# Optimization experiments

Measured on AMD Instinct MI355X. Metric: run time of the kernel, lower is better.

## Reference

```python
import jax, jax.numpy as jnp
import numpy as np

HIDDEN_NF = 256
ATOMICA_DIM = 512
NUM_HEADS = 4
HEAD_DIM = HIDDEN_NF // NUM_HEADS
EDGE_CUTOFF = 10.0
N_LIG = 1024
N_POCKET = 8192
BOX = 30.0  # Angstrom box so the cutoff mask is selective


def _lin(key, fan_in, fan_out):
    kw, kb = jax.random.split(key)
    s = 1.0 / np.sqrt(fan_in)
    W = jax.random.uniform(kw, (fan_in, fan_out), jnp.float32, -s, s)
    b = jax.random.uniform(kb, (fan_out,), jnp.float32, -s, s)
    return W, b


def setup_inputs() -> dict:
    key = jax.random.key(0)
    ks = jax.random.split(key, 12)
    h_lig = jax.random.normal(ks[0], (N_LIG, HIDDEN_NF), jnp.float32)
    x_lig = jax.random.uniform(ks[1], (N_LIG, 3), jnp.float32) * BOX
    h_atomica = jax.random.normal(ks[2], (N_POCKET, ATOMICA_DIM), jnp.float32)
    x_pocket = jax.random.uniform(ks[3], (N_POCKET, 3), jnp.float32) * BOX
    qw, qb = _lin(ks[4], HIDDEN_NF, HIDDEN_NF)
    kw, kb = _lin(ks[5], ATOMICA_DIM, HIDDEN_NF)
    vw, vb = _lin(ks[6], ATOMICA_DIM, HIDDEN_NF)
    ow, ob = _lin(ks[7], HIDDEN_NF, HIDDEN_NF)
    e1w, e1b = _lin(ks[8], 1, HIDDEN_NF)
    e2w, e2b = _lin(ks[9], HIDDEN_NF, NUM_HEADS)
    c1w, c1b = _lin(ks[10], HIDDEN_NF, HIDDEN_NF)
    c2w, c2b = _lin(ks[11], HIDDEN_NF, 1)
    return dict(h_lig=h_lig, x_lig=x_lig, h_atomica=h_atomica, x_pocket=x_pocket,
                qw=qw, qb=qb, kw=kw, kb=kb, vw=vw, vb=vb, ow=ow, ob=ob,
                e1w=e1w, e1b=e1b, e2w=e2w, e2b=e2b,
                c1w=c1w, c1b=c1b, c2w=c2w, c2b=c2b)


def reference(h_lig, x_lig, h_atomica, x_pocket,
              qw, qb, kw, kb, vw, vb, ow, ob,
              e1w, e1b, e2w, e2b, c1w, c1b, c2w, c2b):
    N_lig = h_lig.shape[0]
    silu = jax.nn.silu
    # pairwise geometry: [N_lig, N_pocket, 3]
    rel_pos = x_pocket[None, :, :] - x_lig[:, None, :]
    distances = jnp.linalg.norm(rel_pos, axis=-1, keepdims=True)  # [Nl,Np,1]
    # edge bias MLP: [Nl,Np,num_heads]
    edge_attr = silu(distances @ e1w + e1b) @ e2w + e2b
    mask = distances[..., 0] < EDGE_CUTOFF  # [Nl,Np]
    Q = (h_lig @ qw + qb).reshape(N_lig, NUM_HEADS, HEAD_DIM)
    K = (h_atomica @ kw + kb).reshape(-1, NUM_HEADS, HEAD_DIM)
    V = (h_atomica @ vw + vb).reshape(-1, NUM_HEADS, HEAD_DIM)
    scores = jnp.einsum('ihd,jhd->ijh', Q, K) / np.sqrt(HEAD_DIM).astype(np.float32)
    scores = scores + edge_attr
    scores = jnp.where(mask[..., None], scores, -jnp.inf)
    attn = jax.nn.softmax(scores, axis=1)
    attn = jnp.where(jnp.isnan(attn), 0.0, attn)  # nan_to_num for fully-masked rows
    h_attended = jnp.einsum('ijh,jhd->ihd', attn, V).reshape(N_lig, HIDDEN_NF)
    h_out = h_lig + h_attended @ ow + ob
    # equivariant coordinate update
    normalized_rel_pos = rel_pos / (distances + 1e-8)
    avg_attn = attn.mean(axis=-1, keepdims=True)  # [Nl,Np,1]
    coord_messages = (avg_attn * normalized_rel_pos).sum(axis=1)  # [Nl,3]
    coord_scale = silu(h_attended @ c1w + c1b) @ c2w + c2b  # [Nl,1]
    x_out = x_lig + coord_scale * coord_messages
    return h_out, x_out
```

## Files before the change

kernel.cpp:

```cpp
#include <hip/hip_runtime.h>
#include <hip/hip_bf16.h>


#define NLIG   1024
#define NPOCK  8192
#define HIDDEN 256
#define ADIM   512
#define NHEAD  4
#define HDIM   64
#define NTAB   1024
#define NSPLIT 16
#define CHUNK  (NPOCK / NSPLIT)
#define NT     (CHUNK / 32)
#define LOG2E  1.4426950408889634f
#define QK_SCALE (0.125f * LOG2E)

typedef float f32x16 __attribute__((ext_vector_type(16)));
typedef short short8 __attribute__((ext_vector_type(8)));

union U4S8 { uint4 u; short8 s; };

static __device__ __forceinline__ float exp2h(float x) {
  float r; asm("v_exp_f32 %0, %1" : "=v"(r) : "v"(x)); return r;
}
static __device__ __forceinline__ float rsqh(float x) {
  float r; asm("v_rsq_f32 %0, %1" : "=v"(r) : "v"(x)); return r;
}
static __device__ __forceinline__ unsigned cvtpk(float lo, float hi) {
  unsigned r;
  asm("v_cvt_pk_bf16_f32 %0, %1, %2" : "=v"(r) : "v"(lo), "v"(hi));
  return r;
}
static __device__ __forceinline__ unsigned short f2bf(float f) {
  union { __hip_bfloat16 h; unsigned short u; } c;
  c.h = __float2bfloat16(f);
  return c.u;
}
static __device__ __forceinline__ float bf2f(unsigned u16) {
  union { unsigned uu; float f; } c;
  c.uu = u16 << 16;
  return c.f;
}
static __device__ __forceinline__ short8 load_bf8(const unsigned short* p) {
  U4S8 t; t.u = *(const uint4*)p; return t.s;
}
static __device__ __forceinline__ f32x16 mfma32(short8 a, short8 b, f32x16 c) {
  return __builtin_amdgcn_mfma_f32_32x32x16_bf16(a, b, c, 0, 0, 0);
}
static __device__ __forceinline__ size_t t8(int r, int c, int Cdiv8) {
  return ((size_t)((r >> 5) * Cdiv8 + (c >> 3)) << 8) + ((r & 31) << 3) + (c & 7);
}

#define NCAST 4352
#define NTRANS 448
__global__ __launch_bounds__(256)
void prep_kernel(const float* __restrict__ hA, const float* __restrict__ hl,
                 const float* __restrict__ qw, const float* __restrict__ kw,
                 const float* __restrict__ vw, const float* __restrict__ ow,
                 const float* __restrict__ c1w,
                 const float* __restrict__ e1w, const float* __restrict__ e1b,
                 const float* __restrict__ e2w, const float* __restrict__ e2b,
                 unsigned short* __restrict__ hAb, unsigned short* __restrict__ hlb,
                 unsigned short* __restrict__ qwT, unsigned short* __restrict__ kwT,
                 unsigned short* __restrict__ vwT, unsigned short* __restrict__ owT,
                 unsigned short* __restrict__ c1wT, float* __restrict__ tabG) {
  int bx = blockIdx.x;
  int tid = threadIdx.x;
  if (bx < NCAST) {
    int id = bx * 256 + tid;
    const int nA4 = NPOCK * ADIM / 4;
    if (id < nA4) {
      float4 v = ((const float4*)hA)[id];
      int r = id >> 7, c0 = (id << 2) & 511;
      ushort4 o; o.x = f2bf(v.x); o.y = f2bf(v.y); o.z = f2bf(v.z); o.w = f2bf(v.w);
      *(ushort4*)(hAb + t8(r, c0, 64)) = o;
    } else {
      int j = id - nA4;
      float4 v = ((const float4*)hl)[j];
      int r = j >> 6, c0 = (j << 2) & 255;
      ushort4 o; o.x = f2bf(v.x); o.y = f2bf(v.y); o.z = f2bf(v.z); o.w = f2bf(v.w);
      *(ushort4*)(hlb + t8(r, c0, 32)) = o;
    }
  } else if (bx < NCAST + NTRANS) {
    int b = bx - NCAST;
    const float* src; unsigned short* dst; int K;
    if (b < 64)       { src = qw;  dst = qwT;  K = 256; }
    else if (b < 192) { src = kw;  dst = kwT;  K = 512; b -= 64; }
    else if (b < 320) { src = vw;  dst = vwT;  K = 512; b -= 192; }
    else if (b < 384) { src = ow;  dst = owT;  K = 256; b -= 320; }
    else              { src = c1w; dst = c1wT; K = 256; b -= 384; }
    int kt = K / 32;
    int k0 = (b % kt) * 32, n0 = (b / kt) * 32;
    __shared__ float tile[32][33];
    int tx = tid & 31, ty = tid >> 5;
#pragma unroll
    for (int r = 0; r < 4; ++r)
      tile[ty + 8 * r][tx] = src[(k0 + ty + 8 * r) * 256 + n0 + tx];
    __syncthreads();
#pragma unroll
    for (int r = 0; r < 4; ++r)
      dst[t8(n0 + ty + 8 * r, k0 + tx, K >> 3)] = f2bf(tile[tx][ty + 8 * r]);
  } else {
    int eb = bx - (NCAST + NTRANS);
    int w = tid >> 6, l = tid & 63;
    int entry = eb * 4 + w;
    float d = (entry + 0.5f) * (10.0f / NTAB);
    float a0 = 0.f, a1 = 0.f, a2 = 0.f, a3 = 0.f;
#pragma unroll
    for (int jj = 0; jj < 4; ++jj) {
      int j = l + jj * 64;
      float v = fmaf(d, e1w[j], e1b[j]);
      float s = v / (1.0f + __expf(-v));
      float4 w2 = ((const float4*)e2w)[j];
      a0 = fmaf(s, w2.x, a0);
      a1 = fmaf(s, w2.y, a1);
      a2 = fmaf(s, w2.z, a2);
      a3 = fmaf(s, w2.w, a3);
    }
#pragma unroll
    for (int m = 32; m >= 1; m >>= 1) {
      a0 += __shfl_xor(a0, m); a1 += __shfl_xor(a1, m);
      a2 += __shfl_xor(a2, m); a3 += __shfl_xor(a3, m);
    }
    if (l == 0) {
      tabG[0 * NTAB + entry] = (a0 + e2b[0]) * LOG2E;
      tabG[1 * NTAB + entry] = (a1 + e2b[1]) * LOG2E;
      tabG[2 * NTAB + entry] = (a2 + e2b[2]) * LOG2E;
      tabG[3 * NTAB + entry] = (a3 + e2b[3]) * LOG2E;
    }
  }
}

__global__ __launch_bounds__(256)
void proj_kernel(const unsigned short* __restrict__ hAb, const unsigned short* __restrict__ hlb,
                 const unsigned short* __restrict__ kwT, const unsigned short* __restrict__ vwT,
                 const unsigned short* __restrict__ qwT,
                 const float* __restrict__ kb, const float* __restrict__ vb,
                 const float* __restrict__ qb,
                 unsigned short* __restrict__ Kb, unsigned short* __restrict__ VTb,
                 unsigned short* __restrict__ Qb) {
  int tid = threadIdx.x;
  int w = tid >> 6, lane = tid & 63;
  int lo = lane & 31, hi = lane >> 5;
  int n0 = blockIdx.y * 32;
  int n = n0 + lo;
  if (blockIdx.x < 64) {
    int m0 = blockIdx.x * 128 + w * 32;
    const unsigned short* ap  = hAb + t8(m0 + lo, hi * 8, 64);
    const unsigned short* bkp = kwT + t8(n, hi * 8, 64);
    const unsigned short* bvp = vwT + t8(n, hi * 8, 64);
    f32x16 aK, aV;
#pragma unroll
    for (int i = 0; i < 16; ++i) { aK[i] = 0.f; aV[i] = 0.f; }
#pragma unroll 8
    for (int kk = 0; kk < ADIM / 16; ++kk) {
      short8 a  = load_bf8(ap + kk * 512);
      short8 bk = load_bf8(bkp + kk * 512);
      short8 bv = load_bf8(bvp + kk * 512);
      aK = mfma32(a, bk, aK);
      aV = mfma32(bv, a, aV);
    }
    float bnK = kb[n];
#pragma unroll
    for (int g = 0; g < 4; ++g) {
#pragma unroll
      for (int rr = 0; rr < 4; ++rr) {
        int r = g * 4 + rr;
        int row = g * 8 + hi * 4 + rr;
        Kb[t8(m0 + row, n, 32)] = f2bf(aK[r] + bnK);
        int nv = n0 + row;
        VTb[t8(nv, m0 + lo, 1024)] = f2bf(aV[r] + vb[nv]);
      }
    }
  } else {
    int m0 = (blockIdx.x - 64) * 128 + w * 32;
    const unsigned short* ap = hlb + t8(m0 + lo, hi * 8, 32);
    const unsigned short* bp = qwT + t8(n, hi * 8, 32);
    f32x16 acc;
#pragma unroll
    for (int i = 0; i < 16; ++i) acc[i] = 0.f;
#pragma unroll 8
    for (int kk = 0; kk < HIDDEN / 16; ++kk) {
      short8 a = load_bf8(ap + kk * 512);
      short8 b = load_bf8(bp + kk * 512);
      acc = mfma32(a, b, acc);
    }
    float bn = qb[n];
#pragma unroll
    for (int g = 0; g < 4; ++g) {
#pragma unroll
      for (int rr = 0; rr < 4; ++rr) {
        int r = g * 4 + rr;
        int m = m0 + g * 8 + hi * 4 + rr;
        Qb[t8(m, n, 32)] = f2bf(acc[r] + bn);
      }
    }
  }
}

__global__ __launch_bounds__(256)
void attn_kernel(const unsigned short* __restrict__ Qbf, const unsigned short* __restrict__ Kbf,
                 const unsigned short* __restrict__ VTbf,
                 const float* __restrict__ x_lig, const float* __restrict__ x_pocket,
                 const float* __restrict__ tabG,
                 unsigned* __restrict__ partOb, float4* __restrict__ partZC) {
  __shared__ float4 xch[CHUNK];
  __shared__ float tab[NHEAD][NTAB];

  int tid = threadIdx.x;
  int h = tid >> 6;
  int lane = tid & 63;
  int lo = lane & 31, hi = lane >> 5;
  int qt = blockIdx.x & 31;
  int split = blockIdx.x >> 5;
  int q0 = qt * 32;
  int j0g = split * CHUNK;

  for (int i = tid; i < CHUNK; i += 256) {
    float x = x_pocket[(j0g + i) * 3 + 0];
    float y = x_pocket[(j0g + i) * 3 + 1];
    float z = x_pocket[(j0g + i) * 3 + 2];
    float4 v; v.x = x; v.y = y; v.z = z; v.w = 0.f;
    xch[i] = v;
  }
  for (int i = tid; i < NHEAD * NTAB; i += 256) ((float*)tab)[i] = tabG[i];
  __syncthreads();

  int q = q0 + lo;
  float xl0 = x_lig[q * 3 + 0];
  float xl1 = x_lig[q * 3 + 1];
  float xl2 = x_lig[q * 3 + 2];

  short8 qfr[4];
#pragma unroll
  for (int kk = 0; kk < 4; ++kk)
    qfr[kk] = load_bf8(Qbf + t8(q, h * HDIM + kk * 16 + hi * 8, 32));

  const unsigned short* kbp = Kbf + t8(j0g + lo, h * HDIM + hi * 8, 32);
  const unsigned short* vbp = VTbf + t8(h * HDIM + lo, j0g + hi * 8, 1024);

  f32x16 O0, O1;
#pragma unroll
  for (int i = 0; i < 16; ++i) { O0[i] = 0.f; O1[i] = 0.f; }
  float Z = 0.f, c0 = 0.f, c1 = 0.f, c2 = 0.f;

  short8 kcur[4];
#pragma unroll
  for (int kk = 0; kk < 4; ++kk) kcur[kk] = load_bf8(kbp + kk * 512);

#pragma unroll 1
  for (int t = 0; t < NT; ++t) {
    int jb = t * 32;
    int tn = (t + 1 < NT) ? (t + 1) : t;
    short8 knx0 = load_bf8(kbp + (size_t)tn * 8192 + 0 * 512);
    short8 knx1 = load_bf8(kbp + (size_t)tn * 8192 + 1 * 512);
    short8 knx2 = load_bf8(kbp + (size_t)tn * 8192 + 2 * 512);
    short8 knx3 = load_bf8(kbp + (size_t)tn * 8192 + 3 * 512);
    short8 v00 = load_bf8(vbp + (size_t)t * 1024);
    short8 v01 = load_bf8(vbp + (size_t)t * 1024 + 262144);
    short8 v10 = load_bf8(vbp + (size_t)t * 1024 + 512);
    short8 v11 = load_bf8(vbp + (size_t)t * 1024 + 512 + 262144);

    f32x16 s;
#pragma unroll
    for (int i = 0; i < 16; ++i) s[i] = 0.f;
    s = mfma32(kcur[0], qfr[0], s);
    s = mfma32(kcur[1], qfr[1], s);
    s = mfma32(kcur[2], qfr[2], s);
    s = mfma32(kcur[3], qfr[3], s);

    unsigned wp[8];
    float pprev = 0.f;
#pragma unroll
    for (int r = 0; r < 16; ++r) {
      int jl = (r & 3) + 8 * (r >> 2) + 4 * hi;
      float4 xp = xch[jb + jl];
      float dx = xp.x - xl0, dy = xp.y - xl1, dz = xp.z - xl2;
      float r2 = fmaf(dx, dx, fmaf(dy, dy, dz * dz));
      float r2c = fmaxf(r2, 1e-24f);
      float rinv = rsqh(r2c);
      float d = r2c * rinv;
      int idx = (int)(d * (NTAB / 10.0f));
      idx = idx > (NTAB - 1) ? (NTAB - 1) : idx;
      float b = tab[h][idx];
      float s2 = fmaf(s[r], QK_SCALE, b);
      float pe = (r2 < 100.0f) ? exp2h(s2) : 0.0f;
      Z += pe;
      float pr = pe * rinv;
      c0 = fmaf(pr, dx, c0);
      c1 = fmaf(pr, dy, c1);
      c2 = fmaf(pr, dz, c2);
      if (r & 1) wp[r >> 1] = cvtpk(pprev, pe); else pprev = pe;
    }
    {
      unsigned W0 = wp[0], W1 = wp[1], W2 = wp[2], W3 = wp[3];
      unsigned e01 = (unsigned)__shfl_xor((int)(hi ? W0 : W2), 32);
      unsigned e23 = (unsigned)__shfl_xor((int)(hi ? W1 : W3), 32);
      U4S8 pb;
      pb.u.x = hi ? e01 : W0;
      pb.u.y = hi ? e23 : W1;
      pb.u.z = hi ? W2 : e01;
      pb.u.w = hi ? W3 : e23;
      O0 = mfma32(v00, pb.s, O0);
      O1 = mfma32(v01, pb.s, O1);
    }
    {
      unsigned W0 = wp[4], W1 = wp[5], W2 = wp[6], W3 = wp[7];
      unsigned e01 = (unsigned)__shfl_xor((int)(hi ? W0 : W2), 32);
      unsigned e23 = (unsigned)__shfl_xor((int)(hi ? W1 : W3), 32);
      U4S8 pb;
      pb.u.x = hi ? e01 : W0;
      pb.u.y = hi ? e23 : W1;
      pb.u.z = hi ? W2 : e01;
      pb.u.w = hi ? W3 : e23;
      O0 = mfma32(v10, pb.s, O0);
      O1 = mfma32(v11, pb.s, O1);
    }
    kcur[0] = knx0; kcur[1] = knx1; kcur[2] = knx2; kcur[3] = knx3;
  }

  unsigned* po = partOb + ((size_t)(split * NLIG + q) * (HIDDEN / 2)) + h * (HDIM / 2);
#pragma unroll
  for (int g = 0; g < 4; ++g) {
    uint2 u0;
    u0.x = cvtpk(O0[g * 4 + 0], O0[g * 4 + 1]);
    u0.y = cvtpk(O0[g * 4 + 2], O0[g * 4 + 3]);
    *(uint2*)(po + g * 4 + hi * 2) = u0;
    uint2 u1;
    u1.x = cvtpk(O1[g * 4 + 0], O1[g * 4 + 1]);
    u1.y = cvtpk(O1[g * 4 + 2], O1[g * 4 + 3]);
    *(uint2*)(po + 16 + g * 4 + hi * 2) = u1;
  }
  float Zt = Z + __shfl_xor(Z, 32);
  float c0t = c0 + __shfl_xor(c0, 32);
  float c1t = c1 + __shfl_xor(c1, 32);
  float c2t = c2 + __shfl_xor(c2, 32);
  if (hi == 0) {
    float4 zc; zc.x = Zt; zc.y = c0t; zc.z = c1t; zc.w = c2t;
    partZC[(size_t)(split * NLIG + q) * NHEAD + h] = zc;
  }
}

__global__ __launch_bounds__(256)
void combine_kernel(const unsigned short* __restrict__ partOb, const float4* __restrict__ partZC,
                    unsigned short* __restrict__ hattb, float* __restrict__ cmsg) {
  int q = blockIdx.x;
  int t = threadIdx.x;
  int h = t >> 6;
  float Zh = 0.f;
#pragma unroll
  for (int s = 0; s < NSPLIT; ++s) Zh += partZC[(size_t)(s * NLIG + q) * NHEAD + h].x;
  float o = 0.f;
#pragma unroll
  for (int s = 0; s < NSPLIT; ++s)
    o += bf2f(partOb[(size_t)(s * NLIG + q) * HIDDEN + t]);
  float inv = (Zh > 0.f) ? 1.0f / Zh : 0.f;
  hattb[t8(q, t, 32)] = f2bf(o * inv);

  __shared__ float sm[NHEAD][3];
  if (t < NHEAD) {
    float zz = 0.f, a0 = 0.f, a1 = 0.f, a2 = 0.f;
    for (int s = 0; s < NSPLIT; ++s) {
      float4 v = partZC[(size_t)(s * NLIG + q) * NHEAD + t];
      zz += v.x; a0 += v.y; a1 += v.z; a2 += v.w;
    }
    float iv = (zz > 0.f) ? 0.25f / zz : 0.f;
    sm[t][0] = a0 * iv; sm[t][1] = a1 * iv; sm[t][2] = a2 * iv;
  }
  __syncthreads();
  if (t < 3) cmsg[q * 3 + t] = sm[0][t] + sm[1][t] + sm[2][t] + sm[3][t];
}

__global__ __launch_bounds__(256)
void epi_kernel(const unsigned short* __restrict__ hatt,
                const unsigned short* __restrict__ owT, const unsigned short* __restrict__ c1wT,
                const float* __restrict__ ob, const float* __restrict__ c1b,
                const float* __restrict__ c2w, const float* __restrict__ h_lig,
                float* __restrict__ hout, float* __restrict__ cscale) {
  int tid = threadIdx.x;
  int w = tid >> 6, lane = tid & 63;
  int lo = lane & 31, hi = lane >> 5;
  int m0 = blockIdx.x * 128 + w * 32;
  int n0 = blockIdx.y * 32;
  int n = n0 + lo;
  const unsigned short* ap = hatt + t8(m0 + lo, hi * 8, 32);
  const unsigned short* bo = owT + t8(n, hi * 8, 32);
  const unsigned short* bc = c1wT + t8(n, hi * 8, 32);
  f32x16 aO, aC;
#pragma unroll
  for (int i = 0; i < 16; ++i) { aO[i] = 0.f; aC[i] = 0.f; }
#pragma unroll 8
  for (int kk = 0; kk < HIDDEN / 16; ++kk) {
    short8 a  = load_bf8(ap + kk * 512);
    short8 b1 = load_bf8(bo + kk * 512);
    short8 b2 = load_bf8(bc + kk * 512);
    aO = mfma32(a, b1, aO);
    aC = mfma32(a, b2, aC);
  }
  float obn = ob[n], c1bn = c1b[n], c2wn = c2w[n];
#pragma unroll
  for (int g = 0; g < 4; ++g) {
#pragma unroll
    for (int rr = 0; rr < 4; ++rr) {
      int r = g * 4 + rr;
      int m = m0 + g * 8 + hi * 4 + rr;
      hout[(size_t)m * HIDDEN + n] = aO[r] + obn + h_lig[(size_t)m * HIDDEN + n];
      float v = aC[r] + c1bn;
      float sg = v / (1.0f + exp2h(-LOG2E * v));
      float part = sg * c2wn;
#pragma unroll
      for (int msk = 16; msk >= 1; msk >>= 1) part += __shfl_xor(part, msk);
      if (lo == 0) atomicAdd(&cscale[m], part);
    }
  }
}

__global__ __launch_bounds__(256)
void coordfin_kernel(const float* __restrict__ cscale, const float* __restrict__ c2b,
                     const float* __restrict__ cmsg, const float* __restrict__ x_lig,
                     float* __restrict__ x_out) {
  int id = blockIdx.x * 256 + threadIdx.x;
  if (id < NLIG * 3) {
    int q = id / 3;
    x_out[id] = x_lig[id] + (cscale[q] + c2b[0]) * cmsg[id];
  }
}

extern "C" void kernel_launch(void* const* d_in, const int* in_sizes, int n_in,
                              void* d_out, int out_size, void* d_ws, size_t ws_size,
                              hipStream_t stream) {
  const float* h_lig  = (const float*)d_in[0];
  const float* x_lig  = (const float*)d_in[1];
  const float* h_atom = (const float*)d_in[2];
  const float* x_pock = (const float*)d_in[3];
  const float* qw  = (const float*)d_in[4];
  const float* qb  = (const float*)d_in[5];
  const float* kw  = (const float*)d_in[6];
  const float* kb  = (const float*)d_in[7];
  const float* vw  = (const float*)d_in[8];
  const float* vb  = (const float*)d_in[9];
  const float* ow  = (const float*)d_in[10];
  const float* ob  = (const float*)d_in[11];
  const float* e1w = (const float*)d_in[12];
  const float* e1b = (const float*)d_in[13];
  const float* e2w = (const float*)d_in[14];
  const float* e2b = (const float*)d_in[15];
  const float* c1w = (const float*)d_in[16];
  const float* c1b = (const float*)d_in[17];
  const float* c2w = (const float*)d_in[18];
  const float* c2b = (const float*)d_in[19];

  char* w = (char*)d_ws;
  unsigned short* hAb  = (unsigned short*)w; w += (size_t)NPOCK * ADIM * 2;
  unsigned short* hlb  = (unsigned short*)w; w += (size_t)NLIG * HIDDEN * 2;
  unsigned short* qwT  = (unsigned short*)w; w += 256 * 256 * 2;
  unsigned short* kwT  = (unsigned short*)w; w += 256 * 512 * 2;
  unsigned short* vwT  = (unsigned short*)w; w += 256 * 512 * 2;
  unsigned short* owT  = (unsigned short*)w; w += 256 * 256 * 2;
  unsigned short* c1wT = (unsigned short*)w; w += 256 * 256 * 2;
  unsigned short* Qb   = (unsigned short*)w; w += (size_t)NLIG * HIDDEN * 2;
  unsigned short* Kb   = (unsigned short*)w; w += (size_t)NPOCK * HIDDEN * 2;
  unsigned short* VTb  = (unsigned short*)w; w += (size_t)HIDDEN * NPOCK * 2;
  float* tabG          = (float*)w;          w += NHEAD * NTAB * 4;
  unsigned* partOb     = (unsigned*)w;       w += (size_t)NSPLIT * NLIG * HIDDEN * 2;
  float* partZC        = (float*)w;          w += (size_t)NSPLIT * NLIG * NHEAD * 4 * 4;
  unsigned short* hatt = (unsigned short*)w; w += (size_t)NLIG * HIDDEN * 2;
  float* cmsg          = (float*)w;          w += (size_t)NLIG * 3 * 4;
  float* cscale        = (float*)w;          w += (size_t)NLIG * 4;

  float* hout = (float*)d_out;
  float* xout = ((float*)d_out) + (size_t)NLIG * HIDDEN;

  prep_kernel<<<NCAST + NTRANS + NTAB / 4, 256, 0, stream>>>(
      h_atom, h_lig, qw, kw, vw, ow, c1w, e1w, e1b, e2w, e2b,
      hAb, hlb, qwT, kwT, vwT, owT, c1wT, tabG);
  proj_kernel<<<dim3(72, 8), 256, 0, stream>>>(
      hAb, hlb, kwT, vwT, qwT, kb, vb, qb, Kb, VTb, Qb);
  attn_kernel<<<32 * NSPLIT, 256, 0, stream>>>(Qb, Kb, VTb, x_lig, x_pock, tabG,
                                               partOb, (float4*)partZC);
  combine_kernel<<<NLIG, 256, 0, stream>>>((const unsigned short*)partOb,
                                           (const float4*)partZC, hatt, cmsg);
  hipMemsetAsync(cscale, 0, NLIG * sizeof(float), stream);
  epi_kernel<<<dim3(8, 8), 256, 0, stream>>>(hatt, owT, c1wT, ob, c1b, c2w, h_lig,
                                             hout, cscale);
  coordfin_kernel<<<(NLIG * 3 + 255) / 256, 256, 0, stream>>>(cscale, c2b, cmsg,
                                                              x_lig, xout);
}
```

Baseline: 182.7 us.

## Fuse combine, epilogue and coord kernels; widen projection tiles; tile input cast

```diff
diff --git a/kernel.cpp b/kernel.cpp
--- a/kernel.cpp
+++ b/kernel.cpp
@@ -51,7 +51,8 @@
   return ((size_t)((r >> 5) * Cdiv8 + (c >> 3)) << 8) + ((r & 31) << 3) + (c & 7);
 }
 
-#define NCAST 4352
+#define NCASTA 1024
+#define NCASTL 64
 #define NTRANS 448
 __global__ __launch_bounds__(256)
 void prep_kernel(const float* __restrict__ hA, const float* __restrict__ hl,
@@ -66,23 +67,40 @@
                  unsigned short* __restrict__ c1wT, float* __restrict__ tabG) {
   int bx = blockIdx.x;
   int tid = threadIdx.x;
-  if (bx < NCAST) {
-    int id = bx * 256 + tid;
-    const int nA4 = NPOCK * ADIM / 4;
-    if (id < nA4) {
-      float4 v = ((const float4*)hA)[id];
-      int r = id >> 7, c0 = (id << 2) & 511;
-      ushort4 o; o.x = f2bf(v.x); o.y = f2bf(v.y); o.z = f2bf(v.z); o.w = f2bf(v.w);
-      *(ushort4*)(hAb + t8(r, c0, 64)) = o;
+  if (bx < NCASTA + NCASTL) {
+    const float* src; unsigned short* dst; int stride, Cdiv8, R0, C0;
+    if (bx < NCASTA) {
+      src = hA; dst = hAb; stride = ADIM; Cdiv8 = 64;
+      R0 = (bx >> 3) * 64; C0 = (bx & 7) * 64;
     } else {
-      int j = id - nA4;
-      float4 v = ((const float4*)hl)[j];
-      int r = j >> 6, c0 = (j << 2) & 255;
-      ushort4 o; o.x = f2bf(v.x); o.y = f2bf(v.y); o.z = f2bf(v.z); o.w = f2bf(v.w);
-      *(ushort4*)(hlb + t8(r, c0, 32)) = o;
-    }
-  } else if (bx < NCAST + NTRANS) {
-    int b = bx - NCAST;
+      int b = bx - NCASTA;
+      src = hl; dst = hlb; stride = HIDDEN; Cdiv8 = 32;
+      R0 = (b >> 2) * 64; C0 = (b & 3) * 64;
+    }
+    __shared__ float tf[64][65];
+    int r = tid >> 2;
+#pragma unroll
+    for (int pass = 0; pass < 4; ++pass) {
+      int c4 = (tid & 3) + pass * 4;
+      float4 v = ((const float4*)(src + (size_t)(R0 + r) * stride + C0))[c4];
+      tf[r][c4 * 4 + 0] = v.x; tf[r][c4 * 4 + 1] = v.y;
+      tf[r][c4 * 4 + 2] = v.z; tf[r][c4 * 4 + 3] = v.w;
+    }
+    __syncthreads();
+    unsigned* dstu = (unsigned*)dst;
+    size_t tbase = (size_t)(R0 >> 5) * Cdiv8 + (C0 >> 3);
+#pragma unroll
+    for (int k = 0; k < 8; ++k) {
+      int u = k * 256 + tid;
+      int tile = u >> 7, w2 = u & 127;
+      int rb = tile >> 3, cb = tile & 7;
+      int rr = rb * 32 + (w2 >> 2);
+      int c = cb * 8 + (w2 & 3) * 2;
+      unsigned val = cvtpk(tf[rr][c], tf[rr][c + 1]);
+      dstu[(tbase + (size_t)rb * Cdiv8 + cb) * 128 + w2] = val;
+    }
+  } else if (bx < NCASTA + NCASTL + NTRANS) {
+    int b = bx - (NCASTA + NCASTL);
     const float* src; unsigned short* dst; int K;
     if (b < 64)       { src = qw;  dst = qwT;  K = 256; }
     else if (b < 192) { src = kw;  dst = kwT;  K = 512; b -= 64; }
@@ -101,7 +119,7 @@
     for (int r = 0; r < 4; ++r)
       dst[t8(n0 + ty + 8 * r, k0 + tx, K >> 3)] = f2bf(tile[tx][ty + 8 * r]);
   } else {
-    int eb = bx - (NCAST + NTRANS);
+    int eb = bx - (NCASTA + NCASTL + NTRANS);
     int w = tid >> 6, l = tid & 63;
     int entry = eb * 4 + w;
     float d = (entry + 0.5f) * (10.0f / NTAB);
@@ -142,57 +160,67 @@
   int tid = threadIdx.x;
   int w = tid >> 6, lane = tid & 63;
   int lo = lane & 31, hi = lane >> 5;
-  int n0 = blockIdx.y * 32;
-  int n = n0 + lo;
+  int n0 = blockIdx.y * 64;
   if (blockIdx.x < 64) {
     int m0 = blockIdx.x * 128 + w * 32;
-    const unsigned short* ap  = hAb + t8(m0 + lo, hi * 8, 64);
-    const unsigned short* bkp = kwT + t8(n, hi * 8, 64);
-    const unsigned short* bvp = vwT + t8(n, hi * 8, 64);
-    f32x16 aK, aV;
-#pragma unroll
-    for (int i = 0; i < 16; ++i) { aK[i] = 0.f; aV[i] = 0.f; }
-#pragma unroll 8
+    const unsigned short* ap   = hAb + t8(m0 + lo, hi * 8, 64);
+    const unsigned short* bk0p = kwT + t8(n0 + lo, hi * 8, 64);
+    const unsigned short* bk1p = bk0p + 64 * 256;
+    const unsigned short* bv0p = vwT + t8(n0 + lo, hi * 8, 64);
+    const unsigned short* bv1p = bv0p + 64 * 256;
+    f32x16 aK0, aK1, aV0, aV1;
+#pragma unroll
+    for (int i = 0; i < 16; ++i) { aK0[i] = 0.f; aK1[i] = 0.f; aV0[i] = 0.f; aV1[i] = 0.f; }
+#pragma unroll 4
     for (int kk = 0; kk < ADIM / 16; ++kk) {
-      short8 a  = load_bf8(ap + kk * 512);
-      short8 bk = load_bf8(bkp + kk * 512);
-      short8 bv = load_bf8(bvp + kk * 512);
-      aK = mfma32(a, bk, aK);
-      aV = mfma32(bv, a, aV);
-    }
-    float bnK = kb[n];
+      short8 a   = load_bf8(ap + kk * 512);
+      short8 bk0 = load_bf8(bk0p + kk * 512);
+      short8 bk1 = load_bf8(bk1p + kk * 512);
+      short8 bv0 = load_bf8(bv0p + kk * 512);
+      short8 bv1 = load_bf8(bv1p + kk * 512);
+      aK0 = mfma32(a, bk0, aK0);
+      aK1 = mfma32(a, bk1, aK1);
+      aV0 = mfma32(bv0, a, aV0);
+      aV1 = mfma32(bv1, a, aV1);
+    }
+    float bnK0 = kb[n0 + lo], bnK1 = kb[n0 + 32 + lo];
 #pragma unroll
     for (int g = 0; g < 4; ++g) {
 #pragma unroll
       for (int rr = 0; rr < 4; ++rr) {
         int r = g * 4 + rr;
         int row = g * 8 + hi * 4 + rr;
-        Kb[t8(m0 + row, n, 32)] = f2bf(aK[r] + bnK);
-        int nv = n0 + row;
-        VTb[t8(nv, m0 + lo, 1024)] = f2bf(aV[r] + vb[nv]);
+        Kb[t8(m0 + row, n0 + lo, 32)]      = f2bf(aK0[r] + bnK0);
+        Kb[t8(m0 + row, n0 + 32 + lo, 32)] = f2bf(aK1[r] + bnK1);
+        VTb[t8(n0 + row, m0 + lo, 1024)]      = f2bf(aV0[r] + vb[n0 + row]);
+        VTb[t8(n0 + 32 + row, m0 + lo, 1024)] = f2bf(aV1[r] + vb[n0 + 32 + row]);
       }
     }
   } else {
     int m0 = (blockIdx.x - 64) * 128 + w * 32;
-    const unsigned short* ap = hlb + t8(m0 + lo, hi * 8, 32);
-    const unsigned short* bp = qwT + t8(n, hi * 8, 32);
-    f32x16 acc;
-#pragma unroll
-    for (int i = 0; i < 16; ++i) acc[i] = 0.f;
+    const unsigned short* ap  = hlb + t8(m0 + lo, hi * 8, 32);
+    const unsigned short* b0p = qwT + t8(n0 + lo, hi * 8, 32);
+    const unsigned short* b1p = b0p + 32 * 256;
+    f32x16 a0, a1;
+#pragma unroll
+    for (int i = 0; i < 16; ++i) { a0[i] = 0.f; a1[i] = 0.f; }
 #pragma unroll 8
     for (int kk = 0; kk < HIDDEN / 16; ++kk) {
-      short8 a = load_bf8(ap + kk * 512);
-      short8 b = load_bf8(bp + kk * 512);
-      acc = mfma32(a, b, acc);
-    }
-    float bn = qb[n];
+      short8 a  = load_bf8(ap + kk * 512);
+      short8 b0 = load_bf8(b0p + kk * 512);
+      short8 b1 = load_bf8(b1p + kk * 512);
+      a0 = mfma32(a, b0, a0);
+      a1 = mfma32(a, b1, a1);
+    }
+    float bn0 = qb[n0 + lo], bn1 = qb[n0 + 32 + lo];
 #pragma unroll
     for (int g = 0; g < 4; ++g) {
 #pragma unroll
       for (int rr = 0; rr < 4; ++rr) {
         int r = g * 4 + rr;
         int m = m0 + g * 8 + hi * 4 + rr;
-        Qb[t8(m, n, 32)] = f2bf(acc[r] + bn);
+        Qb[t8(m, n0 + lo, 32)]      = f2bf(a0[r] + bn0);
+        Qb[t8(m, n0 + 32 + lo, 32)] = f2bf(a1[r] + bn1);
       }
     }
   }
@@ -341,61 +369,73 @@
   }
 }
 
-__global__ __launch_bounds__(256)
-void combine_kernel(const unsigned short* __restrict__ partOb, const float4* __restrict__ partZC,
-                    unsigned short* __restrict__ hattb, float* __restrict__ cmsg) {
-  int q = blockIdx.x;
+__global__ __launch_bounds__(512)
+void tail_kernel(const unsigned* __restrict__ partOb, const float4* __restrict__ partZC,
+                 const unsigned short* __restrict__ owT, const unsigned short* __restrict__ c1wT,
+                 const float* __restrict__ ob, const float* __restrict__ c1b,
+                 const float* __restrict__ c2w, const float* __restrict__ c2b,
+                 const float* __restrict__ h_lig, const float* __restrict__ x_lig,
+                 float* __restrict__ hout, float* __restrict__ xout) {
+  __shared__ unsigned hattL[32 * 128];
+  __shared__ float invL[32][4];
+  __shared__ float cmsgL[32][3];
+  __shared__ float cscL[32];
+
   int t = threadIdx.x;
-  int h = t >> 6;
-  float Zh = 0.f;
-#pragma unroll
-  for (int s = 0; s < NSPLIT; ++s) Zh += partZC[(size_t)(s * NLIG + q) * NHEAD + h].x;
-  float o = 0.f;
-#pragma unroll
-  for (int s = 0; s < NSPLIT; ++s)
-    o += bf2f(partOb[(size_t)(s * NLIG + q) * HIDDEN + t]);
-  float inv = (Zh > 0.f) ? 1.0f / Zh : 0.f;
-  hattb[t8(q, t, 32)] = f2bf(o * inv);
-
-  __shared__ float sm[NHEAD][3];
-  if (t < NHEAD) {
+  int q0 = blockIdx.x * 32;
+
+  if (t < 128) {
+    int i = t >> 2, h = t & 3;
     float zz = 0.f, a0 = 0.f, a1 = 0.f, a2 = 0.f;
+#pragma unroll
     for (int s = 0; s < NSPLIT; ++s) {
-      float4 v = partZC[(size_t)(s * NLIG + q) * NHEAD + t];
+      float4 v = partZC[(size_t)(s * NLIG + q0 + i) * NHEAD + h];
       zz += v.x; a0 += v.y; a1 += v.z; a2 += v.w;
     }
+    invL[i][h] = (zz > 0.f) ? 1.0f / zz : 0.f;
     float iv = (zz > 0.f) ? 0.25f / zz : 0.f;
-    sm[t][0] = a0 * iv; sm[t][1] = a1 * iv; sm[t][2] = a2 * iv;
-  }
+    a0 *= iv; a1 *= iv; a2 *= iv;
+    a0 += __shfl_xor(a0, 1); a0 += __shfl_xor(a0, 2);
+    a1 += __shfl_xor(a1, 1); a1 += __shfl_xor(a1, 2);
+    a2 += __shfl_xor(a2, 1); a2 += __shfl_xor(a2, 2);
+    if (h == 0) { cmsgL[i][0] = a0; cmsgL[i][1] = a1; cmsgL[i][2] = a2; }
+  }
+  if (t < 32) cscL[t] = 0.f;
   __syncthreads();
-  if (t < 3) cmsg[q * 3 + t] = sm[0][t] + sm[1][t] + sm[2][t] + sm[3][t];
-}
-
-__global__ __launch_bounds__(256)
-void epi_kernel(const unsigned short* __restrict__ hatt,
-                const unsigned short* __restrict__ owT, const unsigned short* __restrict__ c1wT,
-                const float* __restrict__ ob, const float* __restrict__ c1b,
-                const float* __restrict__ c2w, const float* __restrict__ h_lig,
-                float* __restrict__ hout, float* __restrict__ cscale) {
-  int tid = threadIdx.x;
-  int w = tid >> 6, lane = tid & 63;
+
+  {
+    int c2i = t & 127;
+    int c = c2i * 2;
+#pragma unroll
+    for (int i = t >> 7; i < 32; i += 4) {
+      float o0 = 0.f, o1 = 0.f;
+#pragma unroll
+      for (int s = 0; s < NSPLIT; ++s) {
+        unsigned u = partOb[(size_t)(s * NLIG + q0 + i) * 128 + c2i];
+        o0 += bf2f(u & 0xffffu);
+        o1 += bf2f(u >> 16);
+      }
+      float inv = invL[i][c >> 6];
+      hattL[(c >> 3) * 128 + i * 4 + ((c & 7) >> 1)] = cvtpk(o0 * inv, o1 * inv);
+    }
+  }
+  __syncthreads();
+
+  int w = t >> 6, lane = t & 63;
   int lo = lane & 31, hi = lane >> 5;
-  int m0 = blockIdx.x * 128 + w * 32;
-  int n0 = blockIdx.y * 32;
-  int n = n0 + lo;
-  const unsigned short* ap = hatt + t8(m0 + lo, hi * 8, 32);
+  int n = w * 32 + lo;
   const unsigned short* bo = owT + t8(n, hi * 8, 32);
   const unsigned short* bc = c1wT + t8(n, hi * 8, 32);
   f32x16 aO, aC;
 #pragma unroll
   for (int i = 0; i < 16; ++i) { aO[i] = 0.f; aC[i] = 0.f; }
 #pragma unroll 8
-  for (int kk = 0; kk < HIDDEN / 16; ++kk) {
-    short8 a  = load_bf8(ap + kk * 512);
+  for (int kk = 0; kk < 16; ++kk) {
+    U4S8 av; av.u = *(const uint4*)&hattL[(kk * 2 + hi) * 128 + lo * 4];
     short8 b1 = load_bf8(bo + kk * 512);
     short8 b2 = load_bf8(bc + kk * 512);
-    aO = mfma32(a, b1, aO);
-    aC = mfma32(a, b2, aC);
+    aO = mfma32(av.s, b1, aO);
+    aC = mfma32(av.s, b2, aC);
   }
   float obn = ob[n], c1bn = c1b[n], c2wn = c2w[n];
 #pragma unroll
@@ -403,26 +443,23 @@
 #pragma unroll
     for (int rr = 0; rr < 4; ++rr) {
       int r = g * 4 + rr;
-      int m = m0 + g * 8 + hi * 4 + rr;
+      int mi = g * 8 + hi * 4 + rr;
+      int m = q0 + mi;
       hout[(size_t)m * HIDDEN + n] = aO[r] + obn + h_lig[(size_t)m * HIDDEN + n];
       float v = aC[r] + c1bn;
       float sg = v / (1.0f + exp2h(-LOG2E * v));
       float part = sg * c2wn;
 #pragma unroll
       for (int msk = 16; msk >= 1; msk >>= 1) part += __shfl_xor(part, msk);
-      if (lo == 0) atomicAdd(&cscale[m], part);
-    }
-  }
-}
-
-__global__ __launch_bounds__(256)
-void coordfin_kernel(const float* __restrict__ cscale, const float* __restrict__ c2b,
-                     const float* __restrict__ cmsg, const float* __restrict__ x_lig,
-                     float* __restrict__ x_out) {
-  int id = blockIdx.x * 256 + threadIdx.x;
-  if (id < NLIG * 3) {
-    int q = id / 3;
-    x_out[id] = x_lig[id] + (cscale[q] + c2b[0]) * cmsg[id];
+      if (lo == 0) atomicAdd(&cscL[mi], part);
+    }
+  }
+  __syncthreads();
+
+  if (t < 96) {
+    int i = t / 3, d = t % 3;
+    int q = q0 + i;
+    xout[q * 3 + d] = x_lig[q * 3 + d] + (cscL[i] + c2b[0]) * cmsgL[i][d];
   }
 }
 
@@ -464,25 +501,17 @@
   float* tabG          = (float*)w;          w += NHEAD * NTAB * 4;
   unsigned* partOb     = (unsigned*)w;       w += (size_t)NSPLIT * NLIG * HIDDEN * 2;
   float* partZC        = (float*)w;          w += (size_t)NSPLIT * NLIG * NHEAD * 4 * 4;
-  unsigned short* hatt = (unsigned short*)w; w += (size_t)NLIG * HIDDEN * 2;
-  float* cmsg          = (float*)w;          w += (size_t)NLIG * 3 * 4;
-  float* cscale        = (float*)w;          w += (size_t)NLIG * 4;
 
   float* hout = (float*)d_out;
   float* xout = ((float*)d_out) + (size_t)NLIG * HIDDEN;
 
-  prep_kernel<<<NCAST + NTRANS + NTAB / 4, 256, 0, stream>>>(
+  prep_kernel<<<NCASTA + NCASTL + NTRANS + NTAB / 4, 256, 0, stream>>>(
       h_atom, h_lig, qw, kw, vw, ow, c1w, e1w, e1b, e2w, e2b,
       hAb, hlb, qwT, kwT, vwT, owT, c1wT, tabG);
-  proj_kernel<<<dim3(72, 8), 256, 0, stream>>>(
+  proj_kernel<<<dim3(72, 4), 256, 0, stream>>>(
       hAb, hlb, kwT, vwT, qwT, kb, vb, qb, Kb, VTb, Qb);
   attn_kernel<<<32 * NSPLIT, 256, 0, stream>>>(Qb, Kb, VTb, x_lig, x_pock, tabG,
                                                partOb, (float4*)partZC);
-  combine_kernel<<<NLIG, 256, 0, stream>>>((const unsigned short*)partOb,
-                                           (const float4*)partZC, hatt, cmsg);
-  hipMemsetAsync(cscale, 0, NLIG * sizeof(float), stream);
-  epi_kernel<<<dim3(8, 8), 256, 0, stream>>>(hatt, owT, c1wT, ob, c1b, c2w, h_lig,
-                                             hout, cscale);
-  coordfin_kernel<<<(NLIG * 3 + 255) / 256, 256, 0, stream>>>(cscale, c2b, cmsg,
-                                                              x_lig, xout);
-}
+  tail_kernel<<<32, 512, 0, stream>>>(partOb, (const float4*)partZC, owT, c1wT,
+                                      ob, c1b, c2w, c2b, h_lig, x_lig, hout, xout);
+}
```

New measurement: 183.4 us. Within noise of the previous version (+0.4%).
